# Kernel optimization log

Measured on AMD Instinct MI355X. Metric: run time of the kernel, lower is better.

## Reference

```python
import jax, jax.numpy as jnp
import numpy as np

MARGIN = 0.5
EPS = 1e-5


def setup_inputs() -> dict:
    key = jax.random.key(0)
    k1, k2 = jax.random.split(key)
    n, d, n_new, n_old = 8192, 256, 4096, 4096
    feature = jax.random.normal(k1, (n, d), dtype=jnp.float32)
    target = jax.random.randint(k2, (n,), 0, 100, dtype=jnp.int64)
    new_idx = jnp.arange(n_new, dtype=jnp.int64)
    old_idx = jnp.arange(n_old, dtype=jnp.int64)
    return {"feature": feature, "target": target, "new_idx": new_idx, "old_idx": old_idx}


def _triplet_loss(feature, target, new_idx, old_idx):
    n = feature.shape[0]
    n_new = new_idx.shape[0]
    # alpha switch is based on static shape, exactly as in the torch code
    alpha = 0.9 if old_idx.shape[0] != 0 else 0.5

    sim = feature @ feature.T                      # [n, n]
    sim_new = sim[:, new_idx]                      # [n, n_new]
    t_new = target[new_idx]                        # [n_new]

    same_new = target[:, None] == t_new[None, :]   # [n, n_new]
    is_new_row = jnp.arange(n) < n_new             # [n]

    # positive pairs (only defined for rows i < n_new)
    pos_mask = same_new & (sim_new < 1.0 - EPS)
    pos_loss_new = jnp.sum(jnp.where(pos_mask, 1.0 - sim_new, 0.0), axis=1)  # [n]
    # faithful to the torch bug: rows i >= n_new reuse the stale pos_pair_
    # from the last new row (i = n_new - 1)
    stale_pos = pos_loss_new[n_new - 1]
    pos_loss = jnp.where(is_new_row, pos_loss_new, stale_pos)

    # negatives: new rows scan all columns, old rows scan only new_idx columns
    diff_all = target[:, None] != target[None, :]
    neg_all = jnp.sum(jnp.where(diff_all & (sim > MARGIN), sim, 0.0), axis=1)
    neg_newcols = jnp.sum(jnp.where((~same_new) & (sim_new > MARGIN), sim_new, 0.0), axis=1)
    neg_loss = jnp.where(is_new_row, neg_all, neg_newcols)

    return jnp.mean(alpha * pos_loss + (1.0 - alpha) * neg_loss)


def reference(feature, target, new_idx, old_idx):
    return _triplet_loss(feature, target, new_idx, old_idx)
```

## Files before the change

kernel.cpp:

```cpp
#include <hip/hip_runtime.h>
#include <hip/hip_bf16.h>
#include <stdint.h>

#define MARGIN   0.5f
#define POS_THR  (1.0f - 1e-5f)

typedef __attribute__((ext_vector_type(8))) short  short8;
typedef __attribute__((ext_vector_type(4))) float  f32x4;

#define BM 128
#define BN 128
#define BK 32
#define NPANEL_SHIFT 7

__device__ __forceinline__ ushort f2bf_rne(float x) {
  uint32_t u = __float_as_uint(x);
  u += 0x7fffu + ((u >> 16) & 1u);
  return (ushort)(u >> 16);
}

__device__ __forceinline__ void async_load16(const ushort* g, ushort* l) {
  __builtin_amdgcn_global_load_lds(
      (__attribute__((address_space(1))) void*)(const_cast<ushort*>(g)),
      (__attribute__((address_space(3))) void*)(l),
      16, 0, 0);
}

__global__ void prep_kernel(const float* __restrict__ src, ushort* __restrict__ dst,
                            float* __restrict__ pos, float* __restrict__ neg,
                            int* __restrict__ cnt, int* __restrict__ flags,
                            int total4, int n, int npanel) {
  int i = blockIdx.x * blockDim.x + threadIdx.x;
  if (i < total4) {
    float4 v = reinterpret_cast<const float4*>(src)[i];
    ushort4 o;
    o.x = f2bf_rne(v.x); o.y = f2bf_rne(v.y);
    o.z = f2bf_rne(v.z); o.w = f2bf_rne(v.w);
    reinterpret_cast<ushort4*>(dst)[i] = o;
  }
  if (i < n) { pos[i] = 0.f; neg[i] = 0.f; cnt[i] = 0; }
  if (i < npanel) flags[i] = 0;
}

__global__ void count_kernel(const int* __restrict__ new_idx, int* __restrict__ cnt,
                             int* __restrict__ flags, int n_new) {
  int i = blockIdx.x * blockDim.x + threadIdx.x;
  if (i < n_new) {
    int idx = new_idx[i];
    atomicAdd(&cnt[idx], 1);
    atomicOr(&flags[idx >> NPANEL_SHIFT], 1);
  }
}

__global__ __launch_bounds__(256) void simloss_kernel(
    const ushort* __restrict__ fb, const int* __restrict__ target,
    const int* __restrict__ cnt, const int* __restrict__ colHasNew,
    float* __restrict__ pos_acc, float* __restrict__ neg_acc,
    int d, int n_new) {
  __shared__ __align__(16) ushort Als[3][BM * BK];
  __shared__ __align__(16) ushort Bls[3][BN * BK];
  __shared__ int   t_row[BM];
  __shared__ int   t_col[BN];
  __shared__ float cw_col[BN];

  const int tid = threadIdx.x;
  const int rowBase = blockIdx.y * BM;
  const int colBase = blockIdx.x * BN;

  if (rowBase >= n_new && colHasNew[blockIdx.x] == 0) return;

  if (tid < BM) t_row[tid] = target[rowBase + tid];
  if (tid < BN) {
    t_col[tid]  = target[colBase + tid];
    cw_col[tid] = (float)cnt[colBase + tid];
  }

  const int lane = tid & 63;
  const int wid  = tid >> 6;
  const int wr   = wid >> 1;
  const int wc   = wid & 1;
  const int l15  = lane & 15;
  const int kb   = lane >> 4;

  const int ch0 = (wid * 2 + 0) * 64 + lane;
  const int ch1 = (wid * 2 + 1) * 64 + lane;
  const int r0 = ch0 >> 2, kq0 = (ch0 & 3) ^ ((ch0 >> 3) & 3);
  const int r1 = ch1 >> 2, kq1 = (ch1 & 3) ^ ((ch1 >> 3) & 3);
  const ushort* gA0 = fb + (size_t)(rowBase + r0) * d + kq0 * 8;
  const ushort* gA1 = fb + (size_t)(rowBase + r1) * d + kq1 * 8;
  const ushort* gB0 = fb + (size_t)(colBase + r0) * d + kq0 * 8;
  const ushort* gB1 = fb + (size_t)(colBase + r1) * d + kq1 * 8;
  const int lo0 = (wid * 2 + 0) * 512;
  const int lo1 = (wid * 2 + 1) * 512;

  f32x4 acc[4][4] = {};

  int aoff[4], boff[4];
#pragma unroll
  for (int m = 0; m < 4; ++m) {
    int row = wr * 64 + m * 16 + l15;
    aoff[m] = row * 32 + ((kb ^ ((row >> 1) & 3)) * 8);
  }
#pragma unroll
  for (int nf = 0; nf < 4; ++nf) {
    int row = wc * 64 + nf * 16 + l15;
    boff[nf] = row * 32 + ((kb ^ ((row >> 1) & 3)) * 8);
  }

  asm volatile("s_waitcnt vmcnt(0) lgkmcnt(0)" ::: "memory");
  __builtin_amdgcn_sched_barrier(0);

  async_load16(gA0, &Als[0][lo0]);
  async_load16(gA1, &Als[0][lo1]);
  async_load16(gB0, &Bls[0][lo0]);
  async_load16(gB1, &Bls[0][lo1]);
  const int nk = d / BK;
  if (nk > 1) {
    async_load16(gA0 + BK, &Als[1][lo0]);
    async_load16(gA1 + BK, &Als[1][lo1]);
    async_load16(gB0 + BK, &Bls[1][lo0]);
    async_load16(gB1 + BK, &Bls[1][lo1]);
  }

  int cur = 0;
  for (int t = 0; t < nk; ++t) {
    if (t == nk - 1) asm volatile("s_waitcnt vmcnt(0)" ::: "memory");
    else             asm volatile("s_waitcnt vmcnt(4)" ::: "memory");
    __builtin_amdgcn_s_barrier();
    __builtin_amdgcn_sched_barrier(0);

    if (t + 2 < nk) {
      int nxt = cur + 2; if (nxt >= 3) nxt -= 3;
      int ko = (t + 2) * BK;
      async_load16(gA0 + ko, &Als[nxt][lo0]);
      async_load16(gA1 + ko, &Als[nxt][lo1]);
      async_load16(gB0 + ko, &Bls[nxt][lo0]);
      async_load16(gB1 + ko, &Bls[nxt][lo1]);
    }

    short8 afr[4], bfr[4];
#pragma unroll
    for (int m = 0; m < 4; ++m)
      afr[m] = *reinterpret_cast<const short8*>(&Als[cur][aoff[m]]);
#pragma unroll
    for (int nf = 0; nf < 4; ++nf)
      bfr[nf] = *reinterpret_cast<const short8*>(&Bls[cur][boff[nf]]);
    asm volatile("s_waitcnt lgkmcnt(0)" ::: "memory");
    __builtin_amdgcn_sched_barrier(0);

#pragma unroll
    for (int m = 0; m < 4; ++m)
#pragma unroll
      for (int nf = 0; nf < 4; ++nf)
        acc[m][nf] = __builtin_amdgcn_mfma_f32_16x16x32_bf16(bfr[nf], afr[m], acc[m][nf], 0, 0, 0);

    cur = (cur + 1 == 3) ? 0 : cur + 1;
  }

  int tc_r[4][4]; float cw_r[4][4];
#pragma unroll
  for (int nf = 0; nf < 4; ++nf)
#pragma unroll
    for (int q = 0; q < 4; ++q) {
      int cl = wc * 64 + nf * 16 + kb * 4 + q;
      tc_r[nf][q] = t_col[cl];
      cw_r[nf][q] = cw_col[cl];
    }

#pragma unroll
  for (int m = 0; m < 4; ++m) {
    int rl = wr * 64 + m * 16 + l15;
    int r  = rowBase + rl;
    int tr = t_row[rl];
    bool isnew = (r < n_new);
    float p = 0.f, ng = 0.f;
#pragma unroll
    for (int nf = 0; nf < 4; ++nf)
#pragma unroll
      for (int q = 0; q < 4; ++q) {
        float s = acc[m][nf][q];
        bool same = (tr == tc_r[nf][q]);
        if (isnew) {
          if (same && s < POS_THR)  p  += cw_r[nf][q] * (1.0f - s);
          if (!same && s > MARGIN)  ng += s;
        } else {
          if (!same && s > MARGIN)  ng += cw_r[nf][q] * s;
        }
      }
    p  += __shfl_xor(p, 16);  p  += __shfl_xor(p, 32);
    ng += __shfl_xor(ng, 16); ng += __shfl_xor(ng, 32);
    if (lane < 16) {
      if (p  != 0.f) atomicAdd(&pos_acc[r], p);
      if (ng != 0.f) atomicAdd(&neg_acc[r], ng);
    }
  }
}

__global__ __launch_bounds__(1024) void finalize_kernel(
    const float* __restrict__ pos_acc, const float* __restrict__ neg_acc,
    float* __restrict__ out, int n, int n_new, float alpha) {
  float beta = 1.0f - alpha;
  float local = 0.f;
  int n4 = n >> 2;
  for (int i = threadIdx.x; i < n4; i += blockDim.x) {
    float4 pv = reinterpret_cast<const float4*>(pos_acc)[i];
    float4 nv = reinterpret_cast<const float4*>(neg_acc)[i];
    int r = i * 4;
    local += (r + 0 < n_new) ? alpha * pv.x + beta * nv.x : beta * nv.x;
    local += (r + 1 < n_new) ? alpha * pv.y + beta * nv.y : beta * nv.y;
    local += (r + 2 < n_new) ? alpha * pv.z + beta * nv.z : beta * nv.z;
    local += (r + 3 < n_new) ? alpha * pv.w + beta * nv.w : beta * nv.w;
  }
  if (threadIdx.x == 0 && n > n_new && n_new > 0)
    local += (float)(n - n_new) * alpha * pos_acc[n_new - 1];
#pragma unroll
  for (int off = 32; off; off >>= 1) local += __shfl_xor(local, off);
  __shared__ float red[16];
  int w = threadIdx.x >> 6, ln = threadIdx.x & 63;
  if (ln == 0) red[w] = local;
  __syncthreads();
  if (threadIdx.x == 0) {
    float s = 0.f;
    int nw = blockDim.x >> 6;
    for (int i = 0; i < nw; ++i) s += red[i];
    out[0] = s / (float)n;
  }
}

extern "C" void kernel_launch(void* const* d_in, const int* in_sizes, int n_in,
                              void* d_out, int out_size, void* d_ws, size_t ws_size,
                              hipStream_t stream) {
  const float* feature = (const float*)d_in[0];
  const int*   target  = (const int*)d_in[1];
  const int*   new_idx = (const int*)d_in[2];

  const int n     = in_sizes[1];
  const int d     = in_sizes[0] / n;
  const int n_new = in_sizes[2];
  const int n_old = (n_in > 3) ? in_sizes[3] : 0;
  const float alpha = (n_old != 0) ? 0.9f : 0.5f;
  const int npanel = n / BN;

  auto al = [](size_t x) { return (x + 255) & ~(size_t)255; };
  char* ws = (char*)d_ws;
  ushort* fb      = (ushort*)ws;
  size_t  off     = al((size_t)n * d * sizeof(ushort));
  float*  pos_acc = (float*)(ws + off); off += al((size_t)n * sizeof(float));
  float*  neg_acc = (float*)(ws + off); off += al((size_t)n * sizeof(float));
  int*    cnt     = (int*)(ws + off);   off += al((size_t)n * sizeof(int));
  int*    flags   = (int*)(ws + off);

  int total4 = (n * d) / 4;
  prep_kernel<<<(total4 + 255) / 256, 256, 0, stream>>>(feature, fb, pos_acc,
                                                        neg_acc, cnt, flags,
                                                        total4, n, npanel);
  count_kernel<<<(n_new + 255) / 256, 256, 0, stream>>>(new_idx, cnt, flags, n_new);

  dim3 grid(n / BN, n / BM);
  simloss_kernel<<<grid, 256, 0, stream>>>(fb, target, cnt, flags,
                                           pos_acc, neg_acc, d, n_new);

  finalize_kernel<<<1, 1024, 0, stream>>>(pos_acc, neg_acc, (float*)d_out, n, n_new, alpha);
}
```

Measured before the change: 142.0 us.

## Fuse loss weighting into GEMM epilogue with per-block slot reduction

```diff
diff --git a/kernel.cpp b/kernel.cpp
--- a/kernel.cpp
+++ b/kernel.cpp
@@ -12,6 +12,7 @@
 #define BN 128
 #define BK 32
 #define NPANEL_SHIFT 7
+#define NSLOTS 256
 
 __device__ __forceinline__ ushort f2bf_rne(float x) {
   uint32_t u = __float_as_uint(x);
@@ -27,19 +28,22 @@
 }
 
 __global__ void prep_kernel(const float* __restrict__ src, ushort* __restrict__ dst,
-                            float* __restrict__ pos, float* __restrict__ neg,
                             int* __restrict__ cnt, int* __restrict__ flags,
-                            int total4, int n, int npanel) {
+                            float* __restrict__ misc, int total8, int n, int npanel) {
   int i = blockIdx.x * blockDim.x + threadIdx.x;
-  if (i < total4) {
-    float4 v = reinterpret_cast<const float4*>(src)[i];
-    ushort4 o;
-    o.x = f2bf_rne(v.x); o.y = f2bf_rne(v.y);
-    o.z = f2bf_rne(v.z); o.w = f2bf_rne(v.w);
-    reinterpret_cast<ushort4*>(dst)[i] = o;
-  }
-  if (i < n) { pos[i] = 0.f; neg[i] = 0.f; cnt[i] = 0; }
+  if (i < total8) {
+    const float4* s4 = reinterpret_cast<const float4*>(src);
+    float4 a = s4[i * 2], b = s4[i * 2 + 1];
+    short8 o;
+    o[0] = (short)f2bf_rne(a.x); o[1] = (short)f2bf_rne(a.y);
+    o[2] = (short)f2bf_rne(a.z); o[3] = (short)f2bf_rne(a.w);
+    o[4] = (short)f2bf_rne(b.x); o[5] = (short)f2bf_rne(b.y);
+    o[6] = (short)f2bf_rne(b.z); o[7] = (short)f2bf_rne(b.w);
+    reinterpret_cast<short8*>(dst)[i] = o;
+  }
+  if (i < n) cnt[i] = 0;
   if (i < npanel) flags[i] = 0;
+  if (i < NSLOTS + 1) misc[i] = 0.f;
 }
 
 __global__ void count_kernel(const int* __restrict__ new_idx, int* __restrict__ cnt,
@@ -55,13 +59,13 @@
 __global__ __launch_bounds__(256) void simloss_kernel(
     const ushort* __restrict__ fb, const int* __restrict__ target,
     const int* __restrict__ cnt, const int* __restrict__ colHasNew,
-    float* __restrict__ pos_acc, float* __restrict__ neg_acc,
-    int d, int n_new) {
+    float* __restrict__ misc, int d, int n_new, float alpha) {
   __shared__ __align__(16) ushort Als[3][BM * BK];
   __shared__ __align__(16) ushort Bls[3][BN * BK];
   __shared__ int   t_row[BM];
   __shared__ int   t_col[BN];
   __shared__ float cw_col[BN];
+  __shared__ float red[4];
 
   const int tid = threadIdx.x;
   const int rowBase = blockIdx.y * BM;
@@ -108,7 +112,6 @@
   }
 
   asm volatile("s_waitcnt vmcnt(0) lgkmcnt(0)" ::: "memory");
-  __builtin_amdgcn_sched_barrier(0);
 
   async_load16(gA0, &Als[0][lo0]);
   async_load16(gA1, &Als[0][lo1]);
@@ -126,8 +129,7 @@
   for (int t = 0; t < nk; ++t) {
     if (t == nk - 1) asm volatile("s_waitcnt vmcnt(0)" ::: "memory");
     else             asm volatile("s_waitcnt vmcnt(4)" ::: "memory");
-    __builtin_amdgcn_s_barrier();
-    __builtin_amdgcn_sched_barrier(0);
+    asm volatile("s_barrier" ::: "memory");
 
     if (t + 2 < nk) {
       int nxt = cur + 2; if (nxt >= 3) nxt -= 3;
@@ -145,8 +147,6 @@
 #pragma unroll
     for (int nf = 0; nf < 4; ++nf)
       bfr[nf] = *reinterpret_cast<const short8*>(&Bls[cur][boff[nf]]);
-    asm volatile("s_waitcnt lgkmcnt(0)" ::: "memory");
-    __builtin_amdgcn_sched_barrier(0);
 
 #pragma unroll
     for (int m = 0; m < 4; ++m)
@@ -157,6 +157,7 @@
     cur = (cur + 1 == 3) ? 0 : cur + 1;
   }
 
+  const float beta = 1.0f - alpha;
   int tc_r[4][4]; float cw_r[4][4];
 #pragma unroll
   for (int nf = 0; nf < 4; ++nf)
@@ -167,6 +168,11 @@
       cw_r[nf][q] = cw_col[cl];
     }
 
+  const int  stale_row = n_new - 1;
+  const bool blk_stale = (stale_row >= rowBase) && (stale_row < rowBase + BM);
+  const int  srl = stale_row - rowBase;
+
+  float c = 0.f;
 #pragma unroll
   for (int m = 0; m < 4; ++m) {
     int rl = wr * 64 + m * 16 + l15;
@@ -187,44 +193,31 @@
           if (!same && s > MARGIN)  ng += cw_r[nf][q] * s;
         }
       }
-    p  += __shfl_xor(p, 16);  p  += __shfl_xor(p, 32);
-    ng += __shfl_xor(ng, 16); ng += __shfl_xor(ng, 32);
-    if (lane < 16) {
-      if (p  != 0.f) atomicAdd(&pos_acc[r], p);
-      if (ng != 0.f) atomicAdd(&neg_acc[r], ng);
+    if (blk_stale && wr == (srl >> 6) && m == ((srl >> 4) & 3)) {
+      float pr = p;
+      pr += __shfl_xor(pr, 16); pr += __shfl_xor(pr, 32);
+      if (lane < 16 && rl == srl) atomicAdd(&misc[NSLOTS], pr);
     }
-  }
-}
-
-__global__ __launch_bounds__(1024) void finalize_kernel(
-    const float* __restrict__ pos_acc, const float* __restrict__ neg_acc,
-    float* __restrict__ out, int n, int n_new, float alpha) {
-  float beta = 1.0f - alpha;
-  float local = 0.f;
-  int n4 = n >> 2;
-  for (int i = threadIdx.x; i < n4; i += blockDim.x) {
-    float4 pv = reinterpret_cast<const float4*>(pos_acc)[i];
-    float4 nv = reinterpret_cast<const float4*>(neg_acc)[i];
-    int r = i * 4;
-    local += (r + 0 < n_new) ? alpha * pv.x + beta * nv.x : beta * nv.x;
-    local += (r + 1 < n_new) ? alpha * pv.y + beta * nv.y : beta * nv.y;
-    local += (r + 2 < n_new) ? alpha * pv.z + beta * nv.z : beta * nv.z;
-    local += (r + 3 < n_new) ? alpha * pv.w + beta * nv.w : beta * nv.w;
-  }
-  if (threadIdx.x == 0 && n > n_new && n_new > 0)
-    local += (float)(n - n_new) * alpha * pos_acc[n_new - 1];
-#pragma unroll
-  for (int off = 32; off; off >>= 1) local += __shfl_xor(local, off);
-  __shared__ float red[16];
-  int w = threadIdx.x >> 6, ln = threadIdx.x & 63;
-  if (ln == 0) red[w] = local;
+    c += isnew ? fmaf(alpha, p, beta * ng) : beta * ng;
+  }
+#pragma unroll
+  for (int off = 32; off; off >>= 1) c += __shfl_xor(c, off);
+  if (lane == 0) red[wid] = c;
   __syncthreads();
-  if (threadIdx.x == 0) {
-    float s = 0.f;
-    int nw = blockDim.x >> 6;
-    for (int i = 0; i < nw; ++i) s += red[i];
-    out[0] = s / (float)n;
-  }
+  if (tid == 0)
+    atomicAdd(&misc[(blockIdx.y * gridDim.x + blockIdx.x) & (NSLOTS - 1)],
+              red[0] + red[1] + red[2] + red[3]);
+}
+
+__global__ void finalize_kernel(const float* __restrict__ misc,
+                                float* __restrict__ out, int n, int n_new,
+                                float alpha) {
+  int t = threadIdx.x;
+  float c = misc[t] + misc[t + 64] + misc[t + 128] + misc[t + 192];
+#pragma unroll
+  for (int off = 32; off; off >>= 1) c += __shfl_xor(c, off);
+  if (t == 0)
+    out[0] = (c + (float)(n - n_new) * alpha * misc[NSLOTS]) / (float)n;
 }
 
 extern "C" void kernel_launch(void* const* d_in, const int* in_sizes, int n_in,
@@ -243,22 +236,20 @@
 
   auto al = [](size_t x) { return (x + 255) & ~(size_t)255; };
   char* ws = (char*)d_ws;
-  ushort* fb      = (ushort*)ws;
-  size_t  off     = al((size_t)n * d * sizeof(ushort));
-  float*  pos_acc = (float*)(ws + off); off += al((size_t)n * sizeof(float));
-  float*  neg_acc = (float*)(ws + off); off += al((size_t)n * sizeof(float));
-  int*    cnt     = (int*)(ws + off);   off += al((size_t)n * sizeof(int));
-  int*    flags   = (int*)(ws + off);
-
-  int total4 = (n * d) / 4;
-  prep_kernel<<<(total4 + 255) / 256, 256, 0, stream>>>(feature, fb, pos_acc,
-                                                        neg_acc, cnt, flags,
-                                                        total4, n, npanel);
+  ushort* fb    = (ushort*)ws;
+  size_t  off   = al((size_t)n * d * sizeof(ushort));
+  int*    cnt   = (int*)(ws + off);   off += al((size_t)n * sizeof(int));
+  int*    flags = (int*)(ws + off);   off += al((size_t)npanel * sizeof(int));
+  float*  misc  = (float*)(ws + off);
+
+  int total8 = (n * d) / 8;
+  prep_kernel<<<(total8 + 255) / 256, 256, 0, stream>>>(feature, fb, cnt, flags,
+                                                        misc, total8, n, npanel);
   count_kernel<<<(n_new + 255) / 256, 256, 0, stream>>>(new_idx, cnt, flags, n_new);
 
   dim3 grid(n / BN, n / BM);
-  simloss_kernel<<<grid, 256, 0, stream>>>(fb, target, cnt, flags,
-                                           pos_acc, neg_acc, d, n_new);
-
-  finalize_kernel<<<1, 1024, 0, stream>>>(pos_acc, neg_acc, (float*)d_out, n, n_new, alpha);
-}
+  simloss_kernel<<<grid, 256, 0, stream>>>(fb, target, cnt, flags, misc,
+                                           d, n_new, alpha);
+
+  finalize_kernel<<<1, 64, 0, stream>>>(misc, (float*)d_out, n, n_new, alpha);
+}
```

Result: slower. 152.6 us (+7.4%).
